# Kernel tuning notes

Measured on AMD Instinct MI355X. Metric: run time of the kernel, lower is better.

Reference implementation:

```python
import jax, jax.numpy as jnp
import numpy as np

B, NA, NMAX, NC = 32, 8400, 32, 80
TOPK, ALPHA, BETA, EPS, BG_IDX = 13, 1.0, 6.0, 1e-9, 80
IMG = 640.0


def _ciou(box1, box2, eps=1e-7):
    # box1: (b, nmax, 1, 4) xyxy, box2: (b, 1, na, 4) xyxy -> CIoU (b, nmax, na)
    b1_x1, b1_y1, b1_x2, b1_y2 = (box1[..., 0], box1[..., 1], box1[..., 2], box1[..., 3])
    b2_x1, b2_y1, b2_x2, b2_y2 = (box2[..., 0], box2[..., 1], box2[..., 2], box2[..., 3])
    inter = (jnp.minimum(b1_x2, b2_x2) - jnp.maximum(b1_x1, b2_x1)).clip(0) * \
            (jnp.minimum(b1_y2, b2_y2) - jnp.maximum(b1_y1, b2_y1)).clip(0)
    w1, h1 = b1_x2 - b1_x1, b1_y2 - b1_y1 + eps
    w2, h2 = b2_x2 - b2_x1, b2_y2 - b2_y1 + eps
    union = w1 * h1 + w2 * h2 - inter + eps
    iou = inter / union
    cw = jnp.maximum(b1_x2, b2_x2) - jnp.minimum(b1_x1, b2_x1)
    ch = jnp.maximum(b1_y2, b2_y2) - jnp.minimum(b1_y1, b2_y1)
    c2 = cw * cw + ch * ch + eps
    rho2 = ((b2_x1 + b2_x2 - b1_x1 - b1_x2) ** 2 + (b2_y1 + b2_y2 - b1_y1 - b1_y2) ** 2) / 4.0
    v = (4.0 / np.pi ** 2) * (jnp.arctan(w2 / h2) - jnp.arctan(w1 / h1)) ** 2
    alpha = jax.lax.stop_gradient(v / (v - iou + (1.0 + eps)))
    return iou - (rho2 / c2 + v * alpha)


def _rand_boxes(key, shape):
    # well-formed xyxy boxes inside a 640x640 image
    k1, k2 = jax.random.split(key)
    xy = jax.random.uniform(k1, shape[:-1] + (2,), jnp.float32) * (IMG - 64.0)
    wh = jax.random.uniform(k2, shape[:-1] + (2,), jnp.float32) * 56.0 + 8.0
    return jnp.concatenate([xy, xy + wh], axis=-1)


def setup_inputs() -> dict:
    key = jax.random.key(0)
    ks = jax.random.split(key, 6)
    pd_scores = jax.random.uniform(ks[0], (B, NA, NC), jnp.float32)
    pd_bboxes = _rand_boxes(ks[1], (B, NA, 4))
    anc_points = jax.random.uniform(ks[2], (NA, 2), jnp.float32) * IMG
    gt_labels = jax.random.randint(ks[3], (B, NMAX, 1), 0, NC, dtype=jnp.int32)
    gt_bboxes = _rand_boxes(ks[4], (B, NMAX, 4))
    mask_gt = jnp.ones((B, NMAX, 1), jnp.float32)
    return {"pd_scores": pd_scores, "pd_bboxes": pd_bboxes, "anc_points": anc_points,
            "gt_labels": gt_labels, "gt_bboxes": gt_bboxes, "mask_gt": mask_gt}


def reference(pd_scores, pd_bboxes, anc_points, gt_labels, gt_bboxes, mask_gt):
    b, na, nc = pd_scores.shape
    nmax = gt_bboxes.shape[1]
    # pairwise CIoU between every GT and every predicted box: (b, nmax, na)
    overlaps = _ciou(gt_bboxes[:, :, None, :], pd_bboxes[:, None, :, :])
    # gather predicted class score at each GT's label: (b, nmax, na)
    p = jnp.transpose(pd_scores, (0, 2, 1))                     # (b, nc, na)
    scores = jnp.take_along_axis(p, gt_labels.astype(jnp.int32), axis=1)
    align_metric = (scores ** ALPHA) * (overlaps ** BETA)
    # top-k anchors per GT along the anchor axis, scatter to a boolean mask
    _, topk_idx = jax.lax.top_k(align_metric, TOPK)             # (b, nmax, topk)
    bi = jnp.arange(b)[:, None, None]
    gi = jnp.arange(nmax)[None, :, None]
    mask_pos = jnp.zeros((b, nmax, na), bool).at[bi, gi, topk_idx].set(True)
    target_gt_idx = jnp.argmax(mask_pos, axis=1)                # (b, na)
    fg_mask = mask_pos.sum(axis=1) > 0                          # (b, na)
    # gather assigned GT label / box per anchor
    target_labels = jnp.take_along_axis(gt_labels[..., 0].astype(jnp.int32), target_gt_idx, axis=1)
    target_bboxes = jnp.take_along_axis(gt_bboxes, target_gt_idx[..., None], axis=1)  # (b, na, 4)
    target_scores = jax.nn.one_hot(target_labels, nc, dtype=jnp.float32) * fg_mask[..., None]
    target_labels = jnp.where(fg_mask, target_labels, BG_IDX)
    # normalize target scores by mean positive overlap per anchor, clamped to [0, 1]
    mpf = mask_pos.astype(overlaps.dtype)
    pos_overlaps = jnp.clip((overlaps * mpf).sum(axis=1) / (mpf.sum(axis=1) + EPS), 0.0, 1.0)
    target_scores = target_scores * pos_overlaps[..., None]
    return target_labels, target_bboxes, target_scores, fg_mask, target_gt_idx
```

## Files before the change

### kernel.cpp

```cpp
#include <hip/hip_runtime.h>
#include <math.h>

#define BATCH 32
#define NA 8400
#define NMAX 32
#define NC 80
#define TOPK 13
#define THREADS 256
#define NF4ROW (NA / 4)
#define NPT4 9
#define TILE 128
#define NTILES 66
#define SSTRIDE 81

#define OFF_BOX 268800
#define OFF_SCR 1344000
#define OFF_FG  22848000
#define OFF_TGT 23116800
#define SCR_ELEMS (OFF_FG - OFF_SCR)
#define SCR_F4    (SCR_ELEMS / 4)
#define ZPB_M     2546

typedef float f32x4 __attribute__((ext_vector_type(4)));

__device__ __forceinline__ float ciou_f(float gx1, float gy1, float gx2, float gy2,
                                        float px1, float py1, float px2, float py2) {
    const float eps = 1e-7f;
    float iw = fmaxf(fminf(gx2, px2) - fmaxf(gx1, px1), 0.0f);
    float ih = fmaxf(fminf(gy2, py2) - fmaxf(gy1, py1), 0.0f);
    float inter = iw * ih;
    float w1 = gx2 - gx1, h1 = gy2 - gy1 + eps;
    float w2 = px2 - px1, h2 = py2 - py1 + eps;
    float uni = w1 * h1 + w2 * h2 - inter + eps;
    float iou = inter / uni;
    float cw = fmaxf(gx2, px2) - fminf(gx1, px1);
    float ch = fmaxf(gy2, py2) - fminf(gy1, py1);
    float c2 = cw * cw + ch * ch + eps;
    float dx = px1 + px2 - gx1 - gx2;
    float dy = py1 + py2 - gy1 - gy2;
    float rho2 = (dx * dx + dy * dy) / 4.0f;
    float dd = atanf(w2 / h2) - atanf(w1 / h1);
    float v = (float)(4.0 / (M_PI * M_PI)) * dd * dd;
    float alpha = v / (v - iou + (1.0f + eps));
    return iou - (rho2 / c2 + v * alpha);
}

__global__ __launch_bounds__(THREADS, 3) void metric_kernel(
    const float* __restrict__ pd_scores, const float* __restrict__ pd_bboxes,
    const int* __restrict__ gt_labels, const float* __restrict__ gt_bboxes,
    float* __restrict__ met, unsigned int* __restrict__ mask,
    float* __restrict__ zbase) {
    const int b = blockIdx.y;
    const int abase = blockIdx.x * TILE;
    const int tid = threadIdx.x;
    const int na_tile = min(TILE, NA - abase);
    const float eps = 1e-7f;

    if (tid < na_tile) mask[(size_t)b * NA + abase + tid] = 0u;

    __shared__ float ssc[TILE][SSTRIDE];
    __shared__ float4 spbox[TILE];
    __shared__ float sa2_[TILE], sat2_[TILE];
    __shared__ float sgx1[NMAX], sgy1[NMAX], sgx2[NMAX], sgy2[NMAX];
    __shared__ float sa1[NMAX], sat1[NMAX];
    __shared__ int   slbl[NMAX];

    if (tid < NMAX) {
        float4 g = ((const float4*)gt_bboxes)[b * NMAX + tid];
        float w1 = g.z - g.x, h1 = g.w - g.y + eps;
        sgx1[tid] = g.x; sgy1[tid] = g.y; sgx2[tid] = g.z; sgy2[tid] = g.w;
        sa1[tid]  = w1 * h1;
        sat1[tid] = atanf(w1 / h1);
        slbl[tid] = gt_labels[b * NMAX + tid];
    } else if (tid >= 128) {
        int al = tid - 128;
        if (al < na_tile)
            spbox[al] = ((const float4*)pd_bboxes)[(size_t)b * NA + abase + al];
    }

    const float4* srec4 = (const float4*)(pd_scores + ((size_t)b * NA + abase) * NC);
    const int nf4 = na_tile * 20;
    float4 r[10];
#pragma unroll
    for (int i = 0; i < 10; i++) {
        int f = tid + i * THREADS;
        if (f < nf4) r[i] = srec4[f];
    }
    __syncthreads();

    if (tid < na_tile) {
        float4 p = spbox[tid];
        float w2 = p.z - p.x, h2 = p.w - p.y + eps;
        sa2_[tid]  = w2 * h2;
        sat2_[tid] = atanf(w2 / h2);
    }

#pragma unroll
    for (int i = 0; i < 10; i++) {
        int f = tid + i * THREADS;
        if (f < nf4) {
            int a = f / 20, c = f % 20;
            float* d = &ssc[a][c * 4];
            d[0] = r[i].x; d[1] = r[i].y; d[2] = r[i].z; d[3] = r[i].w;
        }
    }

    if (zbase) {
        const int bid = b * NTILES + blockIdx.x;
        const size_t zoff = (size_t)bid * ZPB_M;
        f32x4* zp = (f32x4*)zbase + zoff;
        const f32x4 z = { 0.f, 0.f, 0.f, 0.f };
#pragma unroll
        for (int i = 0; i < 10; i++) {
            int j = tid + i * THREADS;
            if (j < ZPB_M && zoff + j < SCR_F4)
                zp[j] = z;
        }
    }
    __syncthreads();

    const int q  = tid & 31;
    const int g0 = (tid >> 5) * 4;
    const int a0 = q * 4;
    if (a0 >= na_tile) return;

    float4 P[4]; float A2[4], AT2[4];
#pragma unroll
    for (int j = 0; j < 4; j++) {
        P[j]   = spbox[a0 + j];
        A2[j]  = sa2_[a0 + j];
        AT2[j] = sat2_[a0 + j];
    }

#pragma unroll
    for (int g = 0; g < 4; g++) {
        const int gi = g0 + g;
        const float gx1 = sgx1[gi], gy1 = sgy1[gi], gx2 = sgx2[gi], gy2 = sgy2[gi];
        const float ga1 = sa1[gi], gat1 = sat1[gi];
        const int   lbl = slbl[gi];
        float4 mv;
#pragma unroll
        for (int j = 0; j < 4; j++) {
            float4 p = P[j];
            float iw = fmaxf(fminf(gx2, p.z) - fmaxf(gx1, p.x), 0.0f);
            float ih = fmaxf(fminf(gy2, p.w) - fmaxf(gy1, p.y), 0.0f);
            float inter = iw * ih;
            float uni = ga1 + A2[j] - inter + eps;
            float iou = inter / uni;
            float cw = fmaxf(gx2, p.z) - fminf(gx1, p.x);
            float ch = fmaxf(gy2, p.w) - fminf(gy1, p.y);
            float c2 = cw * cw + ch * ch + eps;
            float dx = p.x + p.z - gx1 - gx2;
            float dy = p.y + p.w - gy1 - gy2;
            float rho2 = (dx * dx + dy * dy) / 4.0f;
            float dd = AT2[j] - gat1;
            float v = (float)(4.0 / (M_PI * M_PI)) * dd * dd;
            float alpha = v / (v - iou + (1.0f + eps));
            float ov = iou - (rho2 / c2 + v * alpha);
            float sc = ssc[a0 + j][lbl];
            float ov2 = ov * ov;
            ((float*)&mv)[j] = sc * (ov2 * ov2 * ov2);
        }
        ((float4*)(met + ((size_t)b * NMAX + gi) * NA + abase))[q] = mv;
    }
}

__global__ __launch_bounds__(THREADS) void topk_kernel(
    const float* __restrict__ met, unsigned int* __restrict__ mask) {
    const int tid  = threadIdx.x;
    const int lane = tid & 63;
    const int w    = tid >> 6;
    const int bid  = blockIdx.x;
    const int b  = bid >> 5;
    const int gi = bid & 31;
    const f32x4* mrow4 = (const f32x4*)(met + ((size_t)b * NMAX + gi) * NA);

    f32x4 m4[NPT4];
#pragma unroll
    for (int j = 0; j < NPT4; j++) {
        int f = j * THREADS + tid;
        if (f < NF4ROW) m4[j] = mrow4[f];
    }

    float bv0 = -INFINITY, bv1 = -INFINITY;
    int   ba0 = 0x7FFFFFFF, ba1 = 0x7FFFFFFF;
#pragma unroll
    for (int j = 0; j < NPT4; j++) {
        int f = j * THREADS + tid;
        bool vf = (f < NF4ROW);
#pragma unroll
        for (int c = 0; c < 4; c++) {
            float v = vf ? m4[j][c] : -INFINITY;
            int   a = vf ? 4 * f + c : 0x7FFFFFFF;
            bool beats0 = (v > bv0) || (v == bv0 && a < ba0);
            bool beats1 = (v > bv1) || (v == bv1 && a < ba1);
            if (beats0) { bv1 = bv0; ba1 = ba0; bv0 = v; ba0 = a; }
            else if (beats1) { bv1 = v; ba1 = a; }
        }
    }
    bool valid1 = true;

    float rv = -INFINITY; int ra = 0x7FFFFFFF;
    for (int k = 0; k < TOPK; k++) {
        float v = bv0; int a = ba0;
#pragma unroll
        for (int s = 1; s < 64; s <<= 1) {
            float ov = __shfl_xor(v, s);
            int   oa = __shfl_xor(a, s);
            if (ov > v || (ov == v && oa < a)) { v = ov; a = oa; }
        }
        if (lane == k) { rv = v; ra = a; }
        if (ba0 == a) {
            if (valid1) { bv0 = bv1; ba0 = ba1; valid1 = false; }
            else {
                float nv = -INFINITY; int na_ = 0x7FFFFFFF;
#pragma unroll
                for (int j = 0; j < NPT4; j++) {
                    int f = j * THREADS + tid;
                    bool vf = (f < NF4ROW);
#pragma unroll
                    for (int c = 0; c < 4; c++) {
                        float mv = vf ? m4[j][c] : -INFINITY;
                        int   ma = vf ? 4 * f + c : 0x7FFFFFFF;
                        bool below = (mv < v) || (mv == v && ma > a);
                        bool beats = (mv > nv) || (mv == nv && ma < na_);
                        if (below && beats && vf) { nv = mv; na_ = ma; }
                    }
                }
                bv0 = nv; ba0 = na_;
            }
        }
    }

    __shared__ float lv[4 * TOPK];
    __shared__ int   la[4 * TOPK];
    if (lane < TOPK) { lv[w * TOPK + lane] = rv; la[w * TOPK + lane] = ra; }
    __syncthreads();

    if (w == 0) {
        float v = (lane < 4 * TOPK) ? lv[lane] : -INFINITY;
        int   a = (lane < 4 * TOPK) ? la[lane] : 0x7FFFFFFF;
        for (int k = 0; k < TOPK; k++) {
            float wv = v; int wa = a;
#pragma unroll
            for (int s = 1; s < 64; s <<= 1) {
                float ov = __shfl_xor(wv, s);
                int   oa = __shfl_xor(wa, s);
                if (ov > wv || (ov == wv && oa < wa)) { wv = ov; wa = oa; }
            }
            if (lane == 0) atomicOr(&mask[(size_t)b * NA + wa], 1u << gi);
            if (a == wa) { v = -INFINITY; a = 0x7FFFFFFF; }
        }
    }
}

__global__ __launch_bounds__(THREADS) void zero_scr_kernel(float* __restrict__ out) {
    f32x4* p = (f32x4*)(out + OFF_SCR);
    const f32x4 z = { 0.f, 0.f, 0.f, 0.f };
    const int stride = gridDim.x * THREADS;
    for (int i = blockIdx.x * THREADS + threadIdx.x; i < SCR_F4; i += stride)
        __builtin_nontemporal_store(z, p + i);
}

__global__ __launch_bounds__(THREADS) void assign_kernel(
    const float* __restrict__ pd_bboxes, const int* __restrict__ gt_labels,
    const float* __restrict__ gt_bboxes, const unsigned int* __restrict__ mask,
    float* __restrict__ out) {
    const int idx = blockIdx.x * THREADS + threadIdx.x;
    const int b = idx / NA;

    unsigned msk = mask[idx];
    int tgt = msk ? (__ffs(msk) - 1) : 0;
    float4 gb = ((const float4*)gt_bboxes)[b * NMAX + tgt];
    int lbl = gt_labels[b * NMAX + tgt];
    float4 p = ((const float4*)pd_bboxes)[idx];

    float sum = 0.0f;
    int cnt = 0;
    unsigned mm = msk;
    while (mm) {
        int i = __ffs(mm) - 1;
        mm &= mm - 1;
        float4 g = ((const float4*)gt_bboxes)[b * NMAX + i];
        sum += ciou_f(g.x, g.y, g.z, g.w, p.x, p.y, p.z, p.w);
        cnt++;
    }
    float po = fminf(fmaxf(sum / ((float)cnt + 1e-9f), 0.0f), 1.0f);

    bool fg = (msk != 0);
    __builtin_nontemporal_store(fg ? (float)lbl : 80.0f, &out[idx]);
    f32x4 gbv = { gb.x, gb.y, gb.z, gb.w };
    __builtin_nontemporal_store(gbv, (f32x4*)(out + OFF_BOX) + idx);
    __builtin_nontemporal_store(fg ? 1.0f : 0.0f, &out[OFF_FG + idx]);
    __builtin_nontemporal_store((float)tgt, &out[OFF_TGT + idx]);
    if (fg) out[OFF_SCR + (size_t)idx * NC + lbl] = po;
}

extern "C" void kernel_launch(void* const* d_in, const int* in_sizes, int n_in,
                              void* d_out, int out_size, void* d_ws, size_t ws_size,
                              hipStream_t stream) {
    const float* pd_scores = (const float*)d_in[0];
    const float* pd_bboxes = (const float*)d_in[1];
    const int*   gt_labels = (const int*)d_in[3];
    const float* gt_bboxes = (const float*)d_in[4];

    float* out = (float*)d_out;
    unsigned int* mask = (unsigned int*)d_ws;

    const size_t MASK_BYTES = (size_t)BATCH * NA * 4;
    const size_t MET_BYTES  = (size_t)BATCH * NMAX * NA * 4;
    const size_t met_off = (MASK_BYTES + 255) & ~(size_t)255;
    const bool ws_met = (ws_size >= met_off + MET_BYTES);

    float* met = ws_met ? (float*)((char*)d_ws + met_off) : out + OFF_SCR;

    dim3 g1(NTILES, BATCH);
    if (ws_met) {
        metric_kernel<<<g1, THREADS, 0, stream>>>(pd_scores, pd_bboxes,
                                                  gt_labels, gt_bboxes, met, mask,
                                                  out + OFF_SCR);
        topk_kernel<<<BATCH * NMAX, THREADS, 0, stream>>>(met, mask);
    } else {
        metric_kernel<<<g1, THREADS, 0, stream>>>(pd_scores, pd_bboxes,
                                                  gt_labels, gt_bboxes, met, mask,
                                                  nullptr);
        topk_kernel<<<BATCH * NMAX, THREADS, 0, stream>>>(met, mask);
        zero_scr_kernel<<<2048, THREADS, 0, stream>>>(out);
    }
    assign_kernel<<<BATCH * NA / THREADS, THREADS, 0, stream>>>(
        pd_bboxes, gt_labels, gt_bboxes, mask, out);
}
```

Before: 79.27 us.

## Compute per-tile top-k candidates in metric kernel and merge them per GT row

The metric kernel now picks a local top-13 per GT row within each 128-anchor tile using wavefront shuffles and writes only (value, index) candidates, rather than writing the full B×NMAX×NA metric matrix. A merge kernel then reduces the 66×13 candidates per row to the final top-k, and zeroing of the score output moves into that merge kernel as nontemporal stores. This is meant to remove the large metric write and re-read and to shrink the top-k scan. In exchange the metric kernel gains a serial 13-step shuffle selection per GT row, with the GT loop no longer unrolled.

```diff
diff --git a/kernel.cpp b/kernel.cpp
--- a/kernel.cpp
+++ b/kernel.cpp
@@ -7,10 +7,9 @@
 #define NC 80
 #define TOPK 13
 #define THREADS 256
-#define NF4ROW (NA / 4)
-#define NPT4 9
 #define TILE 128
 #define NTILES 66
+#define NCAND (NTILES * TOPK)
 #define SSTRIDE 81
 
 #define OFF_BOX 268800
@@ -19,7 +18,7 @@
 #define OFF_TGT 23116800
 #define SCR_ELEMS (OFF_FG - OFF_SCR)
 #define SCR_F4    (SCR_ELEMS / 4)
-#define ZPB_M     2546
+#define ZPB_R     (SCR_F4 / (BATCH * NMAX))
 
 typedef float f32x4 __attribute__((ext_vector_type(4)));
 
@@ -45,13 +44,13 @@
     return iou - (rho2 / c2 + v * alpha);
 }
 
-__global__ __launch_bounds__(THREADS, 3) void metric_kernel(
+__global__ __launch_bounds__(THREADS, 3) void metric_topk_kernel(
     const float* __restrict__ pd_scores, const float* __restrict__ pd_bboxes,
     const int* __restrict__ gt_labels, const float* __restrict__ gt_bboxes,
-    float* __restrict__ met, unsigned int* __restrict__ mask,
-    float* __restrict__ zbase) {
+    float2* __restrict__ cand, unsigned int* __restrict__ mask) {
     const int b = blockIdx.y;
-    const int abase = blockIdx.x * TILE;
+    const int tile = blockIdx.x;
+    const int abase = tile * TILE;
     const int tid = threadIdx.x;
     const int na_tile = min(TILE, NA - abase);
     const float eps = 1e-7f;
@@ -104,99 +103,136 @@
             d[0] = r[i].x; d[1] = r[i].y; d[2] = r[i].z; d[3] = r[i].w;
         }
     }
-
-    if (zbase) {
-        const int bid = b * NTILES + blockIdx.x;
-        const size_t zoff = (size_t)bid * ZPB_M;
-        f32x4* zp = (f32x4*)zbase + zoff;
-        const f32x4 z = { 0.f, 0.f, 0.f, 0.f };
-#pragma unroll
-        for (int i = 0; i < 10; i++) {
-            int j = tid + i * THREADS;
-            if (j < ZPB_M && zoff + j < SCR_F4)
-                zp[j] = z;
-        }
-    }
     __syncthreads();
 
     const int q  = tid & 31;
     const int g0 = (tid >> 5) * 4;
     const int a0 = q * 4;
-    if (a0 >= na_tile) return;
+    const bool avalid = (a0 < na_tile);
 
     float4 P[4]; float A2[4], AT2[4];
-#pragma unroll
-    for (int j = 0; j < 4; j++) {
-        P[j]   = spbox[a0 + j];
-        A2[j]  = sa2_[a0 + j];
-        AT2[j] = sat2_[a0 + j];
-    }
-
-#pragma unroll
+    if (avalid) {
+#pragma unroll
+        for (int j = 0; j < 4; j++) {
+            P[j]   = spbox[a0 + j];
+            A2[j]  = sa2_[a0 + j];
+            AT2[j] = sat2_[a0 + j];
+        }
+    }
+
+#pragma unroll 1
     for (int g = 0; g < 4; g++) {
         const int gi = g0 + g;
         const float gx1 = sgx1[gi], gy1 = sgy1[gi], gx2 = sgx2[gi], gy2 = sgy2[gi];
         const float ga1 = sa1[gi], gat1 = sat1[gi];
         const int   lbl = slbl[gi];
-        float4 mv;
+
+        float mv[4]; int mi[4];
 #pragma unroll
         for (int j = 0; j < 4; j++) {
-            float4 p = P[j];
-            float iw = fmaxf(fminf(gx2, p.z) - fmaxf(gx1, p.x), 0.0f);
-            float ih = fmaxf(fminf(gy2, p.w) - fmaxf(gy1, p.y), 0.0f);
-            float inter = iw * ih;
-            float uni = ga1 + A2[j] - inter + eps;
-            float iou = inter / uni;
-            float cw = fmaxf(gx2, p.z) - fminf(gx1, p.x);
-            float ch = fmaxf(gy2, p.w) - fminf(gy1, p.y);
-            float c2 = cw * cw + ch * ch + eps;
-            float dx = p.x + p.z - gx1 - gx2;
-            float dy = p.y + p.w - gy1 - gy2;
-            float rho2 = (dx * dx + dy * dy) / 4.0f;
-            float dd = AT2[j] - gat1;
-            float v = (float)(4.0 / (M_PI * M_PI)) * dd * dd;
-            float alpha = v / (v - iou + (1.0f + eps));
-            float ov = iou - (rho2 / c2 + v * alpha);
-            float sc = ssc[a0 + j][lbl];
-            float ov2 = ov * ov;
-            ((float*)&mv)[j] = sc * (ov2 * ov2 * ov2);
-        }
-        ((float4*)(met + ((size_t)b * NMAX + gi) * NA + abase))[q] = mv;
-    }
-}
-
-__global__ __launch_bounds__(THREADS) void topk_kernel(
-    const float* __restrict__ met, unsigned int* __restrict__ mask) {
+            if (avalid) {
+                float4 p = P[j];
+                float iw = fmaxf(fminf(gx2, p.z) - fmaxf(gx1, p.x), 0.0f);
+                float ih = fmaxf(fminf(gy2, p.w) - fmaxf(gy1, p.y), 0.0f);
+                float inter = iw * ih;
+                float uni = ga1 + A2[j] - inter + eps;
+                float iou = inter / uni;
+                float cw = fmaxf(gx2, p.z) - fminf(gx1, p.x);
+                float ch = fmaxf(gy2, p.w) - fminf(gy1, p.y);
+                float c2 = cw * cw + ch * ch + eps;
+                float dx = p.x + p.z - gx1 - gx2;
+                float dy = p.y + p.w - gy1 - gy2;
+                float rho2 = (dx * dx + dy * dy) / 4.0f;
+                float dd = AT2[j] - gat1;
+                float v = (float)(4.0 / (M_PI * M_PI)) * dd * dd;
+                float alpha = v / (v - iou + (1.0f + eps));
+                float ov = iou - (rho2 / c2 + v * alpha);
+                float sc = ssc[a0 + j][lbl];
+                float ov2 = ov * ov;
+                mv[j] = sc * (ov2 * ov2 * ov2);
+                mi[j] = abase + a0 + j;
+            } else { mv[j] = -INFINITY; mi[j] = 0x7FFFFFFF; }
+        }
+
+        float v0 = -INFINITY, v1 = -INFINITY;
+        int   i0 = 0x7FFFFFFF, i1 = 0x7FFFFFFF;
+#pragma unroll
+        for (int j = 0; j < 4; j++) {
+            float v = mv[j]; int a = mi[j];
+            bool beats0 = (v > v0) || (v == v0 && a < i0);
+            bool beats1 = (v > v1) || (v == v1 && a < i1);
+            if (beats0) { v1 = v0; i1 = i0; v0 = v; i0 = a; }
+            else if (beats1) { v1 = v; i1 = a; }
+        }
+        bool used1 = false;
+
+        float2* crow = cand + ((size_t)(b * NMAX + gi) * NTILES + tile) * TOPK;
+#pragma unroll 1
+        for (int k = 0; k < TOPK; k++) {
+            float v = v0; int a = i0;
+#pragma unroll
+            for (int s = 1; s < 32; s <<= 1) {
+                float ov = __shfl_xor(v, s);
+                int   oa = __shfl_xor(a, s);
+                if (ov > v || (ov == v && oa < a)) { v = ov; a = oa; }
+            }
+            if (q == k) { float2 e; e.x = v; e.y = __int_as_float(a); crow[k] = e; }
+            if (i0 == a) {
+                if (!used1) { v0 = v1; i0 = i1; used1 = true; }
+                else {
+                    float nv = -INFINITY; int na_ = 0x7FFFFFFF;
+#pragma unroll
+                    for (int j = 0; j < 4; j++) {
+                        float mvj = mv[j]; int mij = mi[j];
+                        bool below = (mvj < v) || (mvj == v && mij > a);
+                        bool beats = (mvj > nv) || (mvj == nv && mij < na_);
+                        if (below && beats) { nv = mvj; na_ = mij; }
+                    }
+                    v0 = nv; i0 = na_;
+                }
+            }
+        }
+    }
+}
+
+__global__ __launch_bounds__(THREADS) void merge_kernel(
+    const float2* __restrict__ cand, unsigned int* __restrict__ mask,
+    float* __restrict__ zbase) {
     const int tid  = threadIdx.x;
     const int lane = tid & 63;
     const int w    = tid >> 6;
-    const int bid  = blockIdx.x;
-    const int b  = bid >> 5;
-    const int gi = bid & 31;
-    const f32x4* mrow4 = (const f32x4*)(met + ((size_t)b * NMAX + gi) * NA);
-
-    f32x4 m4[NPT4];
-#pragma unroll
-    for (int j = 0; j < NPT4; j++) {
-        int f = j * THREADS + tid;
-        if (f < NF4ROW) m4[j] = mrow4[f];
+    const int row  = blockIdx.x;
+    const int b  = row >> 5;
+    const int gi = row & 31;
+    const float2* cr = cand + (size_t)row * NCAND;
+
+    float cv[4]; int ci[4];
+#pragma unroll
+    for (int c = 0; c < 4; c++) {
+        int f = tid + c * THREADS;
+        if (f < NCAND) {
+            float2 e = cr[f];
+            cv[c] = e.x; ci[c] = __float_as_int(e.y);
+        } else { cv[c] = -INFINITY; ci[c] = 0x7FFFFFFF; }
+    }
+
+    if (zbase) {
+        f32x4* zp = (f32x4*)zbase + (size_t)row * ZPB_R;
+        const f32x4 z = { 0.f, 0.f, 0.f, 0.f };
+#pragma unroll 4
+        for (int i = tid; i < ZPB_R; i += THREADS)
+            __builtin_nontemporal_store(z, zp + i);
     }
 
     float bv0 = -INFINITY, bv1 = -INFINITY;
     int   ba0 = 0x7FFFFFFF, ba1 = 0x7FFFFFFF;
 #pragma unroll
-    for (int j = 0; j < NPT4; j++) {
-        int f = j * THREADS + tid;
-        bool vf = (f < NF4ROW);
-#pragma unroll
-        for (int c = 0; c < 4; c++) {
-            float v = vf ? m4[j][c] : -INFINITY;
-            int   a = vf ? 4 * f + c : 0x7FFFFFFF;
-            bool beats0 = (v > bv0) || (v == bv0 && a < ba0);
-            bool beats1 = (v > bv1) || (v == bv1 && a < ba1);
-            if (beats0) { bv1 = bv0; ba1 = ba0; bv0 = v; ba0 = a; }
-            else if (beats1) { bv1 = v; ba1 = a; }
-        }
+    for (int c = 0; c < 4; c++) {
+        float v = cv[c]; int a = ci[c];
+        bool beats0 = (v > bv0) || (v == bv0 && a < ba0);
+        bool beats1 = (v > bv1) || (v == bv1 && a < ba1);
+        if (beats0) { bv1 = bv0; ba1 = ba0; bv0 = v; ba0 = a; }
+        else if (beats1) { bv1 = v; ba1 = a; }
     }
     bool valid1 = true;
 
@@ -215,17 +251,11 @@
             else {
                 float nv = -INFINITY; int na_ = 0x7FFFFFFF;
 #pragma unroll
-                for (int j = 0; j < NPT4; j++) {
-                    int f = j * THREADS + tid;
-                    bool vf = (f < NF4ROW);
-#pragma unroll
-                    for (int c = 0; c < 4; c++) {
-                        float mv = vf ? m4[j][c] : -INFINITY;
-                        int   ma = vf ? 4 * f + c : 0x7FFFFFFF;
-                        bool below = (mv < v) || (mv == v && ma > a);
-                        bool beats = (mv > nv) || (mv == nv && ma < na_);
-                        if (below && beats && vf) { nv = mv; na_ = ma; }
-                    }
+                for (int c = 0; c < 4; c++) {
+                    float mv = cv[c]; int ma = ci[c];
+                    bool below = (mv < v) || (mv == v && ma > a);
+                    bool beats = (mv > nv) || (mv == nv && ma < na_);
+                    if (below && beats) { nv = mv; na_ = ma; }
                 }
                 bv0 = nv; ba0 = na_;
             }
@@ -308,23 +338,20 @@
     unsigned int* mask = (unsigned int*)d_ws;
 
     const size_t MASK_BYTES = (size_t)BATCH * NA * 4;
-    const size_t MET_BYTES  = (size_t)BATCH * NMAX * NA * 4;
-    const size_t met_off = (MASK_BYTES + 255) & ~(size_t)255;
-    const bool ws_met = (ws_size >= met_off + MET_BYTES);
-
-    float* met = ws_met ? (float*)((char*)d_ws + met_off) : out + OFF_SCR;
+    const size_t CAND_BYTES = (size_t)BATCH * NMAX * NCAND * 8;
+    const size_t cand_off = (MASK_BYTES + 255) & ~(size_t)255;
+    const bool ws_cand = (ws_size >= cand_off + CAND_BYTES);
+
+    float2* cand = ws_cand ? (float2*)((char*)d_ws + cand_off)
+                           : (float2*)(out + OFF_SCR);
 
     dim3 g1(NTILES, BATCH);
-    if (ws_met) {
-        metric_kernel<<<g1, THREADS, 0, stream>>>(pd_scores, pd_bboxes,
-                                                  gt_labels, gt_bboxes, met, mask,
-                                                  out + OFF_SCR);
-        topk_kernel<<<BATCH * NMAX, THREADS, 0, stream>>>(met, mask);
+    metric_topk_kernel<<<g1, THREADS, 0, stream>>>(pd_scores, pd_bboxes,
+                                                   gt_labels, gt_bboxes, cand, mask);
+    if (ws_cand) {
+        merge_kernel<<<BATCH * NMAX, THREADS, 0, stream>>>(cand, mask, out + OFF_SCR);
     } else {
-        metric_kernel<<<g1, THREADS, 0, stream>>>(pd_scores, pd_bboxes,
-                                                  gt_labels, gt_bboxes, met, mask,
-                                                  nullptr);
-        topk_kernel<<<BATCH * NMAX, THREADS, 0, stream>>>(met, mask);
+        merge_kernel<<<BATCH * NMAX, THREADS, 0, stream>>>(cand, mask, nullptr);
         zero_scr_kernel<<<2048, THREADS, 0, stream>>>(out);
     }
     assign_kernel<<<BATCH * NA / THREADS, THREADS, 0, stream>>>(
```

Result: slower. 168.6 us (+112.7%).
